# Kernel tuning notes

Hardware: AMD Instinct MI355X
Metric: run time of the kernel (lower is better)

The kernel has to match this reference:

```python
import jax, jax.numpy as jnp
import numpy as np

N_RF = 25   # contour integration RF extent (must be odd, 7-55)
N_CH = 96   # AlexNet conv1 feature maps


def _get_coaligned_masks(weights_type, rf_len, non_overlapping_rfs=True):
    """Faithful numpy replication of the manually-defined coalignment masks."""
    half_rf = rf_len // 2
    kernel = np.zeros((N_CH, rf_len, rf_len), dtype=np.float32)
    step = 3 if non_overlapping_rfs else 1
    pre = list(range(0, half_rf, step))
    post = list(range(half_rf + step, rf_len, step))
    kernel[10, pre, half_rf] = 1
    kernel[10, post, half_rf] = 1
    if weights_type != 'enhance':
        kernel[10, half_rf, pre] = -1
        kernel[10, half_rf, post] = -1
    kernel[5, half_rf, pre] = 1
    kernel[5, half_rf, post] = 1
    if weights_type != 'enhance':
        kernel[5, pre, half_rf] = -1
        kernel[5, post, half_rf] = -1
    kernel[54, (1, 4, 6, 9, 15, 17, 20, 23), (8, 9, 10, 11, 13, 14, 15, 16)] = 1
    kernel[64, list(range(0, half_rf, 3)), list(range(0, half_rf, 3))] = 1
    kernel[64, list(range(half_rf + 3, rf_len, 3)), list(range(half_rf + 3, rf_len, 3))] = 1
    if weights_type != 'enhance':
        kernel[64, list(range(rf_len - 1, half_rf, -3)), list(range(0, half_rf, 3))] = -1
        kernel[64, list(range(half_rf - 3, -1, -3)), list(range(half_rf + 3, rf_len, 3))] = -1
    kernel[67, :, :] = np.copy(kernel[54, :, :])
    kernel[78, (1, 3, 7, 10, 14, 17, 21, 23), (17, 16, 14, 13, 11, 10, 8, 7)] = 1
    return kernel


def setup_inputs() -> dict:
    key = jax.random.key(0)
    x = jax.random.normal(key, (128, 55, 55, N_CH), dtype=jnp.float32)  # NHWC, AlexNet conv1 output
    kernel = jnp.asarray(_get_coaligned_masks('enhance_and_suppress', N_RF))  # [ch, n, n]
    return {"x": x, "kernel": kernel}


def reference(x, kernel):
    # The per-(i,j) python loop in the original is exactly a per-channel (depthwise)
    # cross-correlation with the fixed mask kernel, SAME padding (n//2 each side),
    # followed by (identity) activation and residual add.
    ch = x.shape[-1]
    k = jnp.transpose(kernel, (1, 2, 0))[:, :, None, :]  # [n, n, 1, ch] HWIO depthwise
    lateral = jax.lax.conv_general_dilated(
        x, k,
        window_strides=(1, 1),
        padding='SAME',
        dimension_numbers=('NHWC', 'HWIO', 'NHWC'),
        feature_group_count=ch,
    )
    # activation is linear (None) -> identity
    return lateral + x
```

## Files before the change

### kernel.cpp

```cpp
#include <hip/hip_runtime.h>

#define NCH   96
#define RF    25
#define HALF  12
#define HW    55
#define PLANE (HW * HW)
#define CAP   32
#define MAXA  6
#define SROWS 38
#define LDSW  56

#define WS_META_OFF (NCH * 4 + NCH * CAP * 4 * 2)

__global__ __launch_bounds__(1024) void prep_all(
        const float* __restrict__ kern, int* __restrict__ counts,
        int* __restrict__ tap_off, float* __restrict__ tap_w,
        int* __restrict__ meta) {
    __shared__ int scnt[NCH];
    const int wave = threadIdx.x >> 6;
    const int lane = threadIdx.x & 63;
    for (int c = wave; c < NCH; c += 16) {
        const float* kc = kern + c * (RF * RF);
        int base = 0;
        for (int seg = 0; seg < RF * RF; seg += 64) {
            const int i = seg + lane;
            const float w = (i < RF * RF) ? kc[i] : 0.0f;
            const unsigned long long m = __ballot(w != 0.0f);
            const int pos = base + __popcll(m & ((1ull << lane) - 1ull));
            if (w != 0.0f && pos < CAP) {
                const int dy = i / RF, dx = i - dy * RF;
                tap_off[c * CAP + pos] = (dy << 8) | dx;
                tap_w[c * CAP + pos]   = w;
            }
            base += __popcll(m);
        }
        if (lane == 0) { counts[c] = base; scnt[c] = base; }
    }
    __syncthreads();
    if (threadIdx.x == 0) {
        int na = 0;
        bool fallback = false;
        for (int ch = 0; ch < NCH; ++ch) {
            if (scnt[ch] > 0) {
                if (scnt[ch] > CAP) fallback = true;
                if (na < MAXA) meta[1 + na] = ch;
                ++na;
            }
        }
        if (na > MAXA) fallback = true;
        meta[0] = fallback ? 999 : na;
        for (int a = (na > MAXA ? 0 : na); a < MAXA; ++a) meta[1 + a] = 0;
    }
}

__global__ __launch_bounds__(1024, 8) void contour_tile(
        const float* __restrict__ x, const float* __restrict__ kern,
        const int* __restrict__ counts, const int* __restrict__ tap_off,
        const float* __restrict__ tap_w, const int* __restrict__ meta,
        float* __restrict__ out) {
    __shared__ float sh[MAXA][SROWS][LDSW];
    __shared__ float tw[MAXA][CAP];
    __shared__ int   toff[MAXA][CAP];
    __shared__ int   tcnt[MAXA];
    __shared__ int   chA[MAXA];
    __shared__ signed char c2a[NCH];

    const int tid  = threadIdx.x;
    const int b    = blockIdx.x;
    const int xcd  = b & 7;
    const int s    = b >> 3;
    const int n    = xcd + ((s >> 2) << 3);
    const int q    = s & 3;
    const int y0   = q * 14;
    const int rows = (q < 3) ? 14 : 13;
    const int npx  = rows * HW;

    const float* xn = x   + (size_t)n * (PLANE * NCH);
    float*       on = out + (size_t)n * (PLANE * NCH);

    const int na = meta[0];
    const bool fast = (na <= MAXA);

    if (tid < NCH) c2a[tid] = -1;
    __syncthreads();
    if (fast) {
        if (tid < MAXA) {
            const int c = (tid < na) ? meta[1 + tid] : -1;
            chA[tid]  = c;
            tcnt[tid] = (c >= 0) ? counts[c] : 0;
        }
        if (tid < na) c2a[meta[1 + tid]] = (signed char)tid;
        if (tid >= 64 && tid < 64 + MAXA * CAP) {
            const int a = (tid - 64) / CAP, t = (tid - 64) % CAP;
            const int c = (a < na) ? meta[1 + a] : 0;
            toff[a][t] = tap_off[c * CAP + t];
            tw[a][t]   = tap_w[c * CAP + t];
        }
    }
    __syncthreads();

    {
        const float4* xs = (const float4*)(xn + (size_t)y0 * HW * NCH);
        float4*       os = (float4*)      (on + (size_t)y0 * HW * NCH);
        const int totA = npx * (NCH / 4);
        for (int idx = tid; idx < totA; idx += 1024) {
            const float4 v = xs[idx];
            os[idx] = v;
            if (fast) {
                const int pixel = idx / 24;
                const int g     = idx - pixel * 24;
                const int r     = pixel / HW;
                const int col   = pixel - r * HW;
                const float vv[4] = {v.x, v.y, v.z, v.w};
                #pragma unroll
                for (int kk = 0; kk < 4; ++kk) {
                    const int a = c2a[g * 4 + kk];
                    if (a >= 0) sh[a][r + HALF][col] = vv[kk];
                }
            }
        }
    }

    if (fast) {
        const int totB = na * 24 * HW;
        for (int idx = tid; idx < totB; idx += 1024) {
            const int a   = idx / (24 * HW);
            const int rem = idx - a * (24 * HW);
            const int hs  = rem / HW;
            const int col = rem - hs * HW;
            const int sr  = (hs < HALF) ? hs : hs + rows;
            const int gy  = y0 - HALF + sr;
            float v = 0.0f;
            if ((unsigned)gy < (unsigned)HW)
                v = xn[(size_t)(gy * HW + col) * NCH + chA[a]];
            sh[a][sr][col] = v;
        }
        __syncthreads();

        const int totC = na * npx;
        for (int idx = tid; idx < totC; idx += 1024) {
            const int a   = idx / npx;
            const int rem = idx - a * npx;
            const int r   = rem / HW;
            const int col = rem - r * HW;
            const int cnt = tcnt[a];
            float acc = sh[a][r + HALF][col];
            for (int t = 0; t < cnt; ++t) {
                const int off = toff[a][t];
                const float w = tw[a][t];
                const int dy = off >> 8, dx = off & 255;
                const int xx = col + dx - HALF;
                const bool ok = (unsigned)xx < (unsigned)HW;
                const int  xc = min(max(xx, 0), HW - 1);
                const float v = sh[a][r + dy][xc];
                acc += ok ? w * v : 0.0f;
            }
            on[(size_t)((y0 + r) * HW + col) * NCH + chA[a]] = acc;
        }
    } else {
        for (int idx = tid; idx < npx * (NCH / 4); idx += 1024) {
            const int g   = idx % (NCH / 4);
            const int pix = idx / (NCH / 4);
            const int r   = pix / HW;
            const int col = pix - r * HW;
            const int py  = y0 + r;
            const size_t pbase = (size_t)(py * HW + col) * NCH;
            const float4 xv = *(const float4*)(xn + pbase + g * 4);
            float acc[4] = {xv.x, xv.y, xv.z, xv.w};
            for (int kk = 0; kk < 4; ++kk) {
                const int c = g * 4 + kk;
                const int cnt = counts[c];
                if (cnt == 0) continue;
                float aa = 0.0f;
                if (cnt <= CAP) {
                    for (int t = 0; t < cnt; ++t) {
                        const int off = tap_off[c * CAP + t];
                        const float w = tap_w[c * CAP + t];
                        const int dy = off >> 8, dx = off & 255;
                        const int yy = py + dy - HALF;
                        const int xx = col + dx - HALF;
                        if ((unsigned)yy < (unsigned)HW && (unsigned)xx < (unsigned)HW)
                            aa += w * xn[(size_t)(yy * HW + xx) * NCH + c];
                    }
                } else {
                    for (int dy = 0; dy < RF; ++dy)
                        for (int dx = 0; dx < RF; ++dx) {
                            const float w = kern[(c * RF + dy) * RF + dx];
                            if (w == 0.0f) continue;
                            const int yy = py + dy - HALF;
                            const int xx = col + dx - HALF;
                            if ((unsigned)yy < (unsigned)HW && (unsigned)xx < (unsigned)HW)
                                aa += w * xn[(size_t)(yy * HW + xx) * NCH + c];
                        }
                }
                acc[kk] += aa;
            }
            *(float4*)(on + pbase + g * 4) = make_float4(acc[0], acc[1], acc[2], acc[3]);
        }
    }
}

extern "C" void kernel_launch(void* const* d_in, const int* in_sizes, int n_in,
                              void* d_out, int out_size, void* d_ws, size_t ws_size,
                              hipStream_t stream) {
    const float* x    = (const float*)d_in[0];
    const float* kern = (const float*)d_in[1];
    float* out = (float*)d_out;

    int*   counts  = (int*)d_ws;
    int*   tap_off = (int*)((char*)d_ws + NCH * 4);
    float* tap_w   = (float*)((char*)d_ws + NCH * 4 + NCH * CAP * 4);
    int*   meta    = (int*)((char*)d_ws + WS_META_OFF);

    prep_all<<<1, 1024, 0, stream>>>(kern, counts, tap_off, tap_w, meta);

    contour_tile<<<512, 1024, 0, stream>>>(x, kern, counts, tap_off, tap_w, meta, out);
}
```

Baseline: 384.7 us.

## Stage lateral results in LDS and fuse residual add into single coalesced output pass

Replaces the copy-then-overwrite scheme (full x→out copy plus scattered per-channel strided stores of the lateral sum) with a three-phase flow. Active-channel halo planes are loaded straight from global memory. Lateral sums are computed into a new LDS buffer, and a final float4 pass reads x, adds the staged lateral values for active channels, and writes out once. This removes the duplicate writes and uncoalesced stride-96 stores to the active channels, at the cost of extra LDS (about 18KB) that may lower occupancy. The halo loads become strided gathers for the full 38 rows instead of reusing the interior data from the copy pass.

```diff
diff --git a/kernel.cpp b/kernel.cpp
--- a/kernel.cpp
+++ b/kernel.cpp
@@ -9,6 +9,8 @@
 #define MAXA  6
 #define SROWS 38
 #define LDSW  56
+#define SPLANE (SROWS * HW)
+#define LATP  (14 * HW)
 
 #define WS_META_OFF (NCH * 4 + NCH * CAP * 4 * 2)
 
@@ -59,6 +61,7 @@
         const float* __restrict__ tap_w, const int* __restrict__ meta,
         float* __restrict__ out) {
     __shared__ float sh[MAXA][SROWS][LDSW];
+    __shared__ float latf[MAXA * LATP];
     __shared__ float tw[MAXA][CAP];
     __shared__ int   toff[MAXA][CAP];
     __shared__ int   tcnt[MAXA];
@@ -99,36 +102,13 @@
     }
     __syncthreads();
 
-    {
-        const float4* xs = (const float4*)(xn + (size_t)y0 * HW * NCH);
-        float4*       os = (float4*)      (on + (size_t)y0 * HW * NCH);
-        const int totA = npx * (NCH / 4);
+    if (fast) {
+        const int totA = na * SPLANE;
         for (int idx = tid; idx < totA; idx += 1024) {
-            const float4 v = xs[idx];
-            os[idx] = v;
-            if (fast) {
-                const int pixel = idx / 24;
-                const int g     = idx - pixel * 24;
-                const int r     = pixel / HW;
-                const int col   = pixel - r * HW;
-                const float vv[4] = {v.x, v.y, v.z, v.w};
-                #pragma unroll
-                for (int kk = 0; kk < 4; ++kk) {
-                    const int a = c2a[g * 4 + kk];
-                    if (a >= 0) sh[a][r + HALF][col] = vv[kk];
-                }
-            }
-        }
-    }
-
-    if (fast) {
-        const int totB = na * 24 * HW;
-        for (int idx = tid; idx < totB; idx += 1024) {
-            const int a   = idx / (24 * HW);
-            const int rem = idx - a * (24 * HW);
-            const int hs  = rem / HW;
-            const int col = rem - hs * HW;
-            const int sr  = (hs < HALF) ? hs : hs + rows;
+            const int a   = idx / SPLANE;
+            const int rem = idx - a * SPLANE;
+            const int sr  = rem / HW;
+            const int col = rem - sr * HW;
             const int gy  = y0 - HALF + sr;
             float v = 0.0f;
             if ((unsigned)gy < (unsigned)HW)
@@ -137,14 +117,14 @@
         }
         __syncthreads();
 
-        const int totC = na * npx;
+        const int totC = na * LATP;
         for (int idx = tid; idx < totC; idx += 1024) {
-            const int a   = idx / npx;
-            const int rem = idx - a * npx;
-            const int r   = rem / HW;
-            const int col = rem - r * HW;
+            const int a   = idx / LATP;
+            const int p   = idx - a * LATP;
+            const int r   = p / HW;
+            const int col = p - r * HW;
             const int cnt = tcnt[a];
-            float acc = sh[a][r + HALF][col];
+            float acc = 0.0f;
             for (int t = 0; t < cnt; ++t) {
                 const int off = toff[a][t];
                 const float w = tw[a][t];
@@ -152,10 +132,35 @@
                 const int xx = col + dx - HALF;
                 const bool ok = (unsigned)xx < (unsigned)HW;
                 const int  xc = min(max(xx, 0), HW - 1);
-                const float v = sh[a][r + dy][xc];
-                acc += ok ? w * v : 0.0f;
-            }
-            on[(size_t)((y0 + r) * HW + col) * NCH + chA[a]] = acc;
+                const float vv = sh[a][r + dy][xc];
+                acc += ok ? w * vv : 0.0f;
+            }
+            latf[idx] = acc;
+        }
+        __syncthreads();
+
+        if (tid < 1008) {
+            const int g     = tid % 24;
+            const int pslot = tid / 24;
+            const int a0 = c2a[g * 4 + 0];
+            const int a1 = c2a[g * 4 + 1];
+            const int a2 = c2a[g * 4 + 2];
+            const int a3 = c2a[g * 4 + 3];
+            const bool anyact = (a0 >= 0) | (a1 >= 0) | (a2 >= 0) | (a3 >= 0);
+            const float4* xs = (const float4*)(xn + (size_t)y0 * HW * NCH);
+            float4*       os = (float4*)      (on + (size_t)y0 * HW * NCH);
+            #pragma unroll 2
+            for (int p = pslot; p < npx; p += 42) {
+                const int idx = p * 24 + g;
+                float4 v = xs[idx];
+                if (anyact) {
+                    if (a0 >= 0) v.x += latf[a0 * LATP + p];
+                    if (a1 >= 0) v.y += latf[a1 * LATP + p];
+                    if (a2 >= 0) v.z += latf[a2 * LATP + p];
+                    if (a3 >= 0) v.w += latf[a3 * LATP + p];
+                }
+                os[idx] = v;
+            }
         }
     } else {
         for (int idx = tid; idx < npx * (NCH / 4); idx += 1024) {
```

Measured after the change: 343.8 us. 10.6% less time.
